# Kernel tuning notes

Measured on AMD Instinct MI355X. Metric: run time of the kernel, lower is better.

Reference implementation:

```python
import jax, jax.numpy as jnp
import numpy as np
from jax import lax

KERNEL = 3
EPS = 0.01


def _box_sum(x, k):
    # sum over kxk window, stride 1, SAME-style explicit padding of k//2
    pad = k // 2
    return lax.reduce_window(
        x, 0.0, lax.add,
        window_dimensions=(1, 1, k, k),
        window_strides=(1, 1, 1, 1),
        padding=((0, 0), (0, 0), (pad, pad), (pad, pad)),
    )


def _box_counts(h, w, k, dtype):
    # number of valid (non-padded) elements in each window (count_include_pad=False)
    ones = jnp.ones((1, 1, h, w), dtype=dtype)
    return _box_sum(ones, k)


def _blur(x, counts, k):
    return _box_sum(x, k) / counts


def setup_inputs() -> dict:
    key = jax.random.key(0)
    k1, k2 = jax.random.split(key)
    shape = (8, 16, 512, 512)
    inp = jax.random.normal(k1, shape, dtype=jnp.float32)
    guide = jax.random.normal(k2, shape, dtype=jnp.float32)
    return {"input": inp, "guide": guide}


def reference(input, guide):
    I, p = input, guide
    B, C, H, W = I.shape
    counts = _box_counts(H, W, KERNEL, I.dtype)  # [1,1,H,W]

    mean_I = _blur(I, counts, KERNEL)
    mean_p = _blur(p, counts, KERNEL)
    mean_II = _blur(I * I, counts, KERNEL)
    mean_Ip = _blur(I * p, counts, KERNEL)

    var_I = mean_II - mean_I * mean_I
    cov_Ip = mean_Ip - mean_I * mean_p

    a = cov_Ip / (var_I + EPS)
    b = mean_p - a * mean_I

    mean_a = _blur(a, counts, KERNEL)
    mean_b = _blur(b, counts, KERNEL)

    return mean_a * I + mean_b
```

## Files before the change

kernel.cpp:

```cpp
#include <hip/hip_runtime.h>


constexpr int W  = 512;
constexpr int H  = 512;
constexpr int TW = 64;
constexpr int TH = 16;
constexpr int ABH = TH + 2;
constexpr int ABW = TW + 2;
constexpr float EPS  = 0.01f;
constexpr float INV9 = 1.0f / 9.0f;

template<bool INT>
__device__ __forceinline__ void run_tile(
    const float* __restrict__ Ibase, const float* __restrict__ Pbase,
    float* __restrict__ Obase, int x0, int y0, int tid,
    float2 (*sAB)[ABW])
{
    if (tid < 198) {
        const int s   = tid / 33;
        const int p   = tid - 33 * s;
        const int ay0 = 3 * s;
        const int gx  = x0 - 2 + 2 * p;
        const int gy0 = y0 - 2 + ay0;

        float hI[2][3], hP[2][3], hII[2][3], hIP[2][3];
        #pragma unroll
        for (int j = 0; j < 5; ++j) {
            const int gy = gy0 + j;
            float i0, i1, i2, i3, q0, q1, q2, q3;
            if (INT) {
                const int g = gy * W + gx;
                const float2 a01 = *(const float2*)(Ibase + g);
                const float2 a23 = *(const float2*)(Ibase + g + 2);
                const float2 b01 = *(const float2*)(Pbase + g);
                const float2 b23 = *(const float2*)(Pbase + g + 2);
                i0 = a01.x; i1 = a01.y; i2 = a23.x; i3 = a23.y;
                q0 = b01.x; q1 = b01.y; q2 = b23.x; q3 = b23.y;
            } else {
                i0 = i1 = i2 = i3 = 0.f; q0 = q1 = q2 = q3 = 0.f;
                if ((unsigned)gy < (unsigned)H) {
                    const float* Ir = Ibase + gy * W;
                    const float* Pr = Pbase + gy * W;
                    if (gx >= 0 && gx + 3 < W) {
                        const float2 a01 = *(const float2*)(Ir + gx);
                        const float2 a23 = *(const float2*)(Ir + gx + 2);
                        const float2 b01 = *(const float2*)(Pr + gx);
                        const float2 b23 = *(const float2*)(Pr + gx + 2);
                        i0 = a01.x; i1 = a01.y; i2 = a23.x; i3 = a23.y;
                        q0 = b01.x; q1 = b01.y; q2 = b23.x; q3 = b23.y;
                    } else {
                        if ((unsigned)(gx + 0) < (unsigned)W) { i0 = Ir[gx + 0]; q0 = Pr[gx + 0]; }
                        if ((unsigned)(gx + 1) < (unsigned)W) { i1 = Ir[gx + 1]; q1 = Pr[gx + 1]; }
                        if ((unsigned)(gx + 2) < (unsigned)W) { i2 = Ir[gx + 2]; q2 = Pr[gx + 2]; }
                        if ((unsigned)(gx + 3) < (unsigned)W) { i3 = Ir[gx + 3]; q3 = Pr[gx + 3]; }
                    }
                }
            }
            const int k = j % 3;
            const float tI  = i1 + i2, tP = q1 + q2;
            const float tII = fmaf(i1, i1, i2 * i2);
            const float tIP = fmaf(i1, q1, i2 * q2);
            hI[0][k]  = tI + i0;            hI[1][k]  = tI + i3;
            hP[0][k]  = tP + q0;            hP[1][k]  = tP + q3;
            hII[0][k] = fmaf(i0, i0, tII);  hII[1][k] = fmaf(i3, i3, tII);
            hIP[0][k] = fmaf(i0, q0, tIP);  hIP[1][k] = fmaf(i3, q3, tIP);
            if (j >= 2) {
                const int ay = ay0 + j - 2;
                float ab[4];
                #pragma unroll
                for (int c = 0; c < 2; ++c) {
                    const float wI  = hI[c][0]  + hI[c][1]  + hI[c][2];
                    const float wP  = hP[c][0]  + hP[c][1]  + hP[c][2];
                    const float wII = hII[c][0] + hII[c][1] + hII[c][2];
                    const float wIP = hIP[c][0] + hIP[c][1] + hIP[c][2];
                    float a = 0.f, b = 0.f;
                    if (INT) {
                        const float mI   = wI * INV9, mP = wP * INV9;
                        const float varI = fmaf(-mI, mI, wII * INV9);
                        const float cov  = fmaf(-mI, mP, wIP * INV9);
                        a = cov * __builtin_amdgcn_rcpf(varI + EPS);
                        b = fmaf(-a, mI, mP);
                    } else {
                        const int axg = x0 - 1 + 2 * p + c;
                        const int ayg = y0 - 1 + ay;
                        if ((unsigned)axg < (unsigned)W && (unsigned)ayg < (unsigned)H) {
                            const float cx = 3.f - (float)(axg == 0) - (float)(axg == W - 1);
                            const float cy = 3.f - (float)(ayg == 0) - (float)(ayg == H - 1);
                            const float inv  = __builtin_amdgcn_rcpf(cx * cy);
                            const float mI   = wI * inv, mP = wP * inv;
                            const float varI = fmaf(-mI, mI, wII * inv);
                            const float cov  = fmaf(-mI, mP, wIP * inv);
                            a = cov * __builtin_amdgcn_rcpf(varI + EPS);
                            b = fmaf(-a, mI, mP);
                        }
                    }
                    ab[2 * c] = a; ab[2 * c + 1] = b;
                }
                *(float4*)&sAB[ay][2 * p] = make_float4(ab[0], ab[1], ab[2], ab[3]);
            }
        }
    }
    __syncthreads();

    {
        const int q   = tid & 31;
        const int r   = tid >> 5;
        const int ox0 = 2 * q;
        const int oy0 = 2 * r;
        float hA[2][3], hB[2][3];
        #pragma unroll
        for (int j = 0; j < 4; ++j) {
            const float4 c01 = *(const float4*)&sAB[oy0 + j][ox0];
            const float4 c23 = *(const float4*)&sAB[oy0 + j][ox0 + 2];
            const float a0 = c01.x, b0 = c01.y, a1 = c01.z, b1 = c01.w;
            const float a2 = c23.x, b2 = c23.y, a3 = c23.z, b3 = c23.w;
            const int k = j % 3;
            const float tA = a1 + a2, tB = b1 + b2;
            hA[0][k] = tA + a0; hA[1][k] = tA + a3;
            hB[0][k] = tB + b0; hB[1][k] = tB + b3;
            if (j >= 2) {
                const int oy = oy0 + j - 2;
                const int gy = y0 + oy;
                const int go = gy * W + x0 + ox0;
                const float2 iv = *(const float2*)(Ibase + go);
                float res[2];
                #pragma unroll
                for (int c = 0; c < 2; ++c) {
                    const float sa = hA[c][0] + hA[c][1] + hA[c][2];
                    const float sb = hB[c][0] + hB[c][1] + hB[c][2];
                    float inv;
                    if (INT) {
                        inv = INV9;
                    } else {
                        const int gxo = x0 + ox0 + c;
                        const float cx = 3.f - (float)(gxo == 0) - (float)(gxo == W - 1);
                        const float cy = 3.f - (float)(gy == 0) - (float)(gy == H - 1);
                        inv = __builtin_amdgcn_rcpf(cx * cy);
                    }
                    const float Ic = (c == 0) ? iv.x : iv.y;
                    res[c] = fmaf(sa * inv, Ic, sb * inv);
                }
                *(float2*)(Obase + go) = make_float2(res[0], res[1]);
            }
        }
    }
}

__global__ __launch_bounds__(256, 8) void guide_filter_kernel(
    const float* __restrict__ I, const float* __restrict__ P,
    float* __restrict__ O)
{
    __shared__ __align__(16) float2 sAB[ABH][ABW];

    const int tid = threadIdx.x;
    const int x0  = blockIdx.x * TW;
    const int y0  = blockIdx.y * TH;
    const size_t img_off = (size_t)blockIdx.z * (size_t)(W * H);
    const bool interior = (blockIdx.x > 0) & (blockIdx.x < gridDim.x - 1) &
                          (blockIdx.y > 0) & (blockIdx.y < gridDim.y - 1);
    if (interior) {
        run_tile<true >(I + img_off, P + img_off, (float*)O + img_off, x0, y0, tid, sAB);
    } else {
        run_tile<false>(I + img_off, P + img_off, (float*)O + img_off, x0, y0, tid, sAB);
    }
}

extern "C" void kernel_launch(void* const* d_in, const int* in_sizes, int n_in,
                              void* d_out, int out_size, void* d_ws, size_t ws_size,
                              hipStream_t stream) {
    const float* I = (const float*)d_in[0];
    const float* P = (const float*)d_in[1];
    float*       O = (float*)d_out;
    const int images = in_sizes[0] / (W * H);
    dim3 grid(W / TW, H / TH, images);
    guide_filter_kernel<<<grid, dim3(256), 0, stream>>>(I, P, O);
}
```

Measured before the change: 358.2 us.

## Replace shared-memory tiles with register-streaming column strips using wave shuffles

Each wavefront now processes a 128-column strip (120 output columns) and streams 64 rows downward, keeping rolling 3-row box sums for the statistics and for a/b in registers. Horizontal neighbours come from lane shuffles instead of a shared-memory tile, which removes the LDS staging, the block barrier and most halo re-reads. In exchange the grid is much smaller, there is a long serial per-row dependency chain, and the shuffles and boundary masks add per-row work.

```diff
diff --git a/kernel.cpp b/kernel.cpp
--- a/kernel.cpp
+++ b/kernel.cpp
@@ -1,168 +1,115 @@
 #include <hip/hip_runtime.h>
 
 
-constexpr int W  = 512;
-constexpr int H  = 512;
-constexpr int TW = 64;
-constexpr int TH = 16;
-constexpr int ABH = TH + 2;
-constexpr int ABW = TW + 2;
-constexpr float EPS  = 0.01f;
-constexpr float INV9 = 1.0f / 9.0f;
+constexpr int W = 512, H = 512;
+constexpr int OUTW = 120;
+constexpr int RG_H = 64;
+constexpr float EPS = 0.01f;
 
-template<bool INT>
-__device__ __forceinline__ void run_tile(
-    const float* __restrict__ Ibase, const float* __restrict__ Pbase,
-    float* __restrict__ Obase, int x0, int y0, int tid,
-    float2 (*sAB)[ABW])
-{
-    if (tid < 198) {
-        const int s   = tid / 33;
-        const int p   = tid - 33 * s;
-        const int ay0 = 3 * s;
-        const int gx  = x0 - 2 + 2 * p;
-        const int gy0 = y0 - 2 + ay0;
+#define GF_AB_COL(cx, wI, wP, wII, wIP, aa, bb)                               \
+    {                                                                         \
+        const float inv = __builtin_amdgcn_rcpf((cx) * cyA);                  \
+        const float mI = (wI) * inv, mP = (wP) * inv;                         \
+        const float varI = fmaf(-mI, mI, (wII) * inv);                        \
+        const float cov  = fmaf(-mI, mP, (wIP) * inv);                        \
+        aa = cov * __builtin_amdgcn_rcpf(varI + EPS);                         \
+        bb = fmaf(-aa, mI, mP);                                               \
+    }
 
-        float hI[2][3], hP[2][3], hII[2][3], hIP[2][3];
-        #pragma unroll
-        for (int j = 0; j < 5; ++j) {
-            const int gy = gy0 + j;
-            float i0, i1, i2, i3, q0, q1, q2, q3;
-            if (INT) {
-                const int g = gy * W + gx;
-                const float2 a01 = *(const float2*)(Ibase + g);
-                const float2 a23 = *(const float2*)(Ibase + g + 2);
-                const float2 b01 = *(const float2*)(Pbase + g);
-                const float2 b23 = *(const float2*)(Pbase + g + 2);
-                i0 = a01.x; i1 = a01.y; i2 = a23.x; i3 = a23.y;
-                q0 = b01.x; q1 = b01.y; q2 = b23.x; q3 = b23.y;
-            } else {
-                i0 = i1 = i2 = i3 = 0.f; q0 = q1 = q2 = q3 = 0.f;
-                if ((unsigned)gy < (unsigned)H) {
-                    const float* Ir = Ibase + gy * W;
-                    const float* Pr = Pbase + gy * W;
-                    if (gx >= 0 && gx + 3 < W) {
-                        const float2 a01 = *(const float2*)(Ir + gx);
-                        const float2 a23 = *(const float2*)(Ir + gx + 2);
-                        const float2 b01 = *(const float2*)(Pr + gx);
-                        const float2 b23 = *(const float2*)(Pr + gx + 2);
-                        i0 = a01.x; i1 = a01.y; i2 = a23.x; i3 = a23.y;
-                        q0 = b01.x; q1 = b01.y; q2 = b23.x; q3 = b23.y;
-                    } else {
-                        if ((unsigned)(gx + 0) < (unsigned)W) { i0 = Ir[gx + 0]; q0 = Pr[gx + 0]; }
-                        if ((unsigned)(gx + 1) < (unsigned)W) { i1 = Ir[gx + 1]; q1 = Pr[gx + 1]; }
-                        if ((unsigned)(gx + 2) < (unsigned)W) { i2 = Ir[gx + 2]; q2 = Pr[gx + 2]; }
-                        if ((unsigned)(gx + 3) < (unsigned)W) { i3 = Ir[gx + 3]; q3 = Pr[gx + 3]; }
-                    }
-                }
-            }
-            const int k = j % 3;
-            const float tI  = i1 + i2, tP = q1 + q2;
-            const float tII = fmaf(i1, i1, i2 * i2);
-            const float tIP = fmaf(i1, q1, i2 * q2);
-            hI[0][k]  = tI + i0;            hI[1][k]  = tI + i3;
-            hP[0][k]  = tP + q0;            hP[1][k]  = tP + q3;
-            hII[0][k] = fmaf(i0, i0, tII);  hII[1][k] = fmaf(i3, i3, tII);
-            hIP[0][k] = fmaf(i0, q0, tIP);  hIP[1][k] = fmaf(i3, q3, tIP);
-            if (j >= 2) {
-                const int ay = ay0 + j - 2;
-                float ab[4];
-                #pragma unroll
-                for (int c = 0; c < 2; ++c) {
-                    const float wI  = hI[c][0]  + hI[c][1]  + hI[c][2];
-                    const float wP  = hP[c][0]  + hP[c][1]  + hP[c][2];
-                    const float wII = hII[c][0] + hII[c][1] + hII[c][2];
-                    const float wIP = hIP[c][0] + hIP[c][1] + hIP[c][2];
-                    float a = 0.f, b = 0.f;
-                    if (INT) {
-                        const float mI   = wI * INV9, mP = wP * INV9;
-                        const float varI = fmaf(-mI, mI, wII * INV9);
-                        const float cov  = fmaf(-mI, mP, wIP * INV9);
-                        a = cov * __builtin_amdgcn_rcpf(varI + EPS);
-                        b = fmaf(-a, mI, mP);
-                    } else {
-                        const int axg = x0 - 1 + 2 * p + c;
-                        const int ayg = y0 - 1 + ay;
-                        if ((unsigned)axg < (unsigned)W && (unsigned)ayg < (unsigned)H) {
-                            const float cx = 3.f - (float)(axg == 0) - (float)(axg == W - 1);
-                            const float cy = 3.f - (float)(ayg == 0) - (float)(ayg == H - 1);
-                            const float inv  = __builtin_amdgcn_rcpf(cx * cy);
-                            const float mI   = wI * inv, mP = wP * inv;
-                            const float varI = fmaf(-mI, mI, wII * inv);
-                            const float cov  = fmaf(-mI, mP, wIP * inv);
-                            a = cov * __builtin_amdgcn_rcpf(varI + EPS);
-                            b = fmaf(-a, mI, mP);
-                        }
-                    }
-                    ab[2 * c] = a; ab[2 * c + 1] = b;
-                }
-                *(float4*)&sAB[ay][2 * p] = make_float4(ab[0], ab[1], ab[2], ab[3]);
-            }
-        }
-    }
-    __syncthreads();
+#define GF_STEP(r, S, SP1)                                                    \
+  {                                                                           \
+    const int gy = oy0 - 2 + (r);                                             \
+    const bool yok = (unsigned)gy < (unsigned)H;                              \
+    float ix = 0.f, iy = 0.f, px = 0.f, py = 0.f;                             \
+    if (xok & yok) {                                                          \
+        const float2 vi = *(const float2*)(Ib + gy * W + c0);                 \
+        const float2 vp = *(const float2*)(Pb + gy * W + c0);                 \
+        ix = vi.x; iy = vi.y; px = vp.x; py = vp.y;                           \
+    }                                                                         \
+    const float iLy = __shfl(iy, lm1);                                        \
+    const float pLy = __shfl(py, lm1);                                        \
+    const float iRx = __shfl(ix, lp1);                                        \
+    const float pRx = __shfl(px, lp1);                                        \
+    const float cI = ix + iy, cP = px + py;                                   \
+    hI0[S] = cI + iLy;  hI1[S] = cI + iRx;                                    \
+    hP0[S] = cP + pLy;  hP1[S] = cP + pRx;                                    \
+    const float cII = fmaf(ix, ix, iy * iy);                                  \
+    const float cIP = fmaf(ix, px, iy * py);                                  \
+    hII0[S] = fmaf(iLy, iLy, cII);  hII1[S] = fmaf(iRx, iRx, cII);            \
+    hIP0[S] = fmaf(iLy, pLy, cIP);  hIP1[S] = fmaf(iRx, pRx, cIP);            \
+    iC0[S] = ix; iC1[S] = iy;                                                 \
+    const int ay = gy - 1;                                                    \
+    const float cyA = 3.f - (float)(ay == 0) - (float)(ay == H - 1);          \
+    const bool abok = xok & ((unsigned)ay < (unsigned)H);                     \
+    float a0, b0, a1, b1;                                                     \
+    GF_AB_COL(cx0, hI0[0] + hI0[1] + hI0[2], hP0[0] + hP0[1] + hP0[2],        \
+              hII0[0] + hII0[1] + hII0[2], hIP0[0] + hIP0[1] + hIP0[2],       \
+              a0, b0)                                                         \
+    GF_AB_COL(cx1, hI1[0] + hI1[1] + hI1[2], hP1[0] + hP1[1] + hP1[2],        \
+              hII1[0] + hII1[1] + hII1[2], hIP1[0] + hIP1[1] + hIP1[2],       \
+              a1, b1)                                                         \
+    a0 = abok ? a0 : 0.f;  b0 = abok ? b0 : 0.f;                              \
+    a1 = abok ? a1 : 0.f;  b1 = abok ? b1 : 0.f;                              \
+    const float aLy = __shfl(a1, lm1);                                        \
+    const float bLy = __shfl(b1, lm1);                                        \
+    const float aRx = __shfl(a0, lp1);                                        \
+    const float bRx = __shfl(b0, lp1);                                        \
+    const float cA = a0 + a1, cB = b0 + b1;                                   \
+    hA0[S] = cA + aLy;  hA1[S] = cA + aRx;                                    \
+    hB0[S] = cB + bLy;  hB1[S] = cB + bRx;                                    \
+    if ((r) >= 4) {                                                           \
+        const int oy = gy - 2;                                                \
+        const float cyO = 3.f - (float)(oy == 0) - (float)(oy == H - 1);      \
+        const float q0 = __builtin_amdgcn_rcpf(cx0 * cyO);                    \
+        const float q1 = __builtin_amdgcn_rcpf(cx1 * cyO);                    \
+        const float sA0 = hA0[0] + hA0[1] + hA0[2];                           \
+        const float sB0 = hB0[0] + hB0[1] + hB0[2];                           \
+        const float sA1 = hA1[0] + hA1[1] + hA1[2];                           \
+        const float sB1 = hB1[0] + hB1[1] + hB1[2];                           \
+        const float o0 = fmaf(sA0 * q0, iC0[SP1], sB0 * q0);                  \
+        const float o1 = fmaf(sA1 * q1, iC1[SP1], sB1 * q1);                  \
+        if (stok) *(float2*)(Ob + oy * W + c0) = make_float2(o0, o1);         \
+    }                                                                         \
+  }
 
-    {
-        const int q   = tid & 31;
-        const int r   = tid >> 5;
-        const int ox0 = 2 * q;
-        const int oy0 = 2 * r;
-        float hA[2][3], hB[2][3];
-        #pragma unroll
-        for (int j = 0; j < 4; ++j) {
-            const float4 c01 = *(const float4*)&sAB[oy0 + j][ox0];
-            const float4 c23 = *(const float4*)&sAB[oy0 + j][ox0 + 2];
-            const float a0 = c01.x, b0 = c01.y, a1 = c01.z, b1 = c01.w;
-            const float a2 = c23.x, b2 = c23.y, a3 = c23.z, b3 = c23.w;
-            const int k = j % 3;
-            const float tA = a1 + a2, tB = b1 + b2;
-            hA[0][k] = tA + a0; hA[1][k] = tA + a3;
-            hB[0][k] = tB + b0; hB[1][k] = tB + b3;
-            if (j >= 2) {
-                const int oy = oy0 + j - 2;
-                const int gy = y0 + oy;
-                const int go = gy * W + x0 + ox0;
-                const float2 iv = *(const float2*)(Ibase + go);
-                float res[2];
-                #pragma unroll
-                for (int c = 0; c < 2; ++c) {
-                    const float sa = hA[c][0] + hA[c][1] + hA[c][2];
-                    const float sb = hB[c][0] + hB[c][1] + hB[c][2];
-                    float inv;
-                    if (INT) {
-                        inv = INV9;
-                    } else {
-                        const int gxo = x0 + ox0 + c;
-                        const float cx = 3.f - (float)(gxo == 0) - (float)(gxo == W - 1);
-                        const float cy = 3.f - (float)(gy == 0) - (float)(gy == H - 1);
-                        inv = __builtin_amdgcn_rcpf(cx * cy);
-                    }
-                    const float Ic = (c == 0) ? iv.x : iv.y;
-                    res[c] = fmaf(sa * inv, Ic, sb * inv);
-                }
-                *(float2*)(Obase + go) = make_float2(res[0], res[1]);
-            }
-        }
-    }
-}
-
-__global__ __launch_bounds__(256, 8) void guide_filter_kernel(
+__global__ __launch_bounds__(256, 4) void guide_filter_kernel(
     const float* __restrict__ I, const float* __restrict__ P,
     float* __restrict__ O)
 {
-    __shared__ __align__(16) float2 sAB[ABH][ABW];
+    const int lane = threadIdx.x & 63;
+    const int wid  = threadIdx.x >> 6;
+    const int band = blockIdx.x;
+    const int rg   = blockIdx.y * 4 + wid;
+    const size_t img_off = (size_t)blockIdx.z * (size_t)(W * H);
+    const float* Ib = I + img_off;
+    const float* Pb = P + img_off;
+    float*       Ob = O + img_off;
 
-    const int tid = threadIdx.x;
-    const int x0  = blockIdx.x * TW;
-    const int y0  = blockIdx.y * TH;
-    const size_t img_off = (size_t)blockIdx.z * (size_t)(W * H);
-    const bool interior = (blockIdx.x > 0) & (blockIdx.x < gridDim.x - 1) &
-                          (blockIdx.y > 0) & (blockIdx.y < gridDim.y - 1);
-    if (interior) {
-        run_tile<true >(I + img_off, P + img_off, (float*)O + img_off, x0, y0, tid, sAB);
-    } else {
-        run_tile<false>(I + img_off, P + img_off, (float*)O + img_off, x0, y0, tid, sAB);
+    const int c0 = band * OUTW - 2 + 2 * lane;
+    const int c1 = c0 + 1;
+    const bool xok  = (unsigned)c0 < (unsigned)W;
+    const bool stok = xok & (lane >= 1) & (lane <= 60);
+    const float cx0 = 3.f - (float)(c0 == 0);
+    const float cx1 = 3.f - (float)(c1 == W - 1);
+    const int oy0 = rg * RG_H;
+    const int lm1 = lane - 1, lp1 = lane + 1;
+
+    float hI0[3], hI1[3], hP0[3], hP1[3], hII0[3], hII1[3], hIP0[3], hIP1[3];
+    float hA0[3], hA1[3], hB0[3], hB1[3], iC0[3], iC1[3];
+    #pragma unroll
+    for (int s = 0; s < 3; ++s) {
+        hI0[s]=hI1[s]=hP0[s]=hP1[s]=hII0[s]=hII1[s]=hIP0[s]=hIP1[s]=0.f;
+        hA0[s]=hA1[s]=hB0[s]=hB1[s]=iC0[s]=iC1[s]=0.f;
     }
+
+    for (int g = 0; g < 22; ++g) {
+        const int r = 3 * g;
+        GF_STEP(r,     0, 1)
+        GF_STEP(r + 1, 1, 2)
+        GF_STEP(r + 2, 2, 0)
+    }
+    GF_STEP(66, 0, 1)
+    GF_STEP(67, 1, 2)
 }
 
 extern "C" void kernel_launch(void* const* d_in, const int* in_sizes, int n_in,
@@ -172,6 +119,6 @@
     const float* P = (const float*)d_in[1];
     float*       O = (float*)d_out;
     const int images = in_sizes[0] / (W * H);
-    dim3 grid(W / TW, H / TH, images);
+    dim3 grid(5, 2, images);
     guide_filter_kernel<<<grid, dim3(256), 0, stream>>>(I, P, O);
 }
```

New measurement: 332.0 us. -7.3%, faster.

## Stage input halo in LDS and double-buffer across four horizontal tiles per block

Applied to the files above, without the earlier changes.

Each block now walks four consecutive 64-wide tiles. For each tile it loads the interleaved I/P halo into a double-buffered shared-memory array using clamped coalesced loads, and prefetches the next tile into registers while the current one is computed. Stage 2 reads from LDS instead of issuing overlapping global loads, which removes redundant global traffic and divergent boundary loads. In exchange the block uses more LDS and gets a smaller grid (launch bounds drop to 4), with added barriers per tile and possible occupancy loss.

```diff
diff --git a/kernel.cpp b/kernel.cpp
--- a/kernel.cpp
+++ b/kernel.cpp
@@ -1,61 +1,31 @@
 #include <hip/hip_runtime.h>
 
 
-constexpr int W  = 512;
-constexpr int H  = 512;
-constexpr int TW = 64;
-constexpr int TH = 16;
+constexpr int W  = 512, H = 512;
+constexpr int TW = 64,  TH = 16, NT = 4;
+constexpr int IPH = TH + 4;
+constexpr int IPW = TW + 4;
 constexpr int ABH = TH + 2;
 constexpr int ABW = TW + 2;
 constexpr float EPS  = 0.01f;
 constexpr float INV9 = 1.0f / 9.0f;
 
 template<bool INT>
-__device__ __forceinline__ void run_tile(
-    const float* __restrict__ Ibase, const float* __restrict__ Pbase,
-    float* __restrict__ Obase, int x0, int y0, int tid,
-    float2 (*sAB)[ABW])
+__device__ __forceinline__ void stage2(
+    const float2 (*sIPb)[IPW], float2 (*sAB)[ABW], int x0, int y0, int tid)
 {
     if (tid < 198) {
         const int s   = tid / 33;
         const int p   = tid - 33 * s;
         const int ay0 = 3 * s;
-        const int gx  = x0 - 2 + 2 * p;
-        const int gy0 = y0 - 2 + ay0;
-
         float hI[2][3], hP[2][3], hII[2][3], hIP[2][3];
         #pragma unroll
         for (int j = 0; j < 5; ++j) {
-            const int gy = gy0 + j;
-            float i0, i1, i2, i3, q0, q1, q2, q3;
-            if (INT) {
-                const int g = gy * W + gx;
-                const float2 a01 = *(const float2*)(Ibase + g);
-                const float2 a23 = *(const float2*)(Ibase + g + 2);
-                const float2 b01 = *(const float2*)(Pbase + g);
-                const float2 b23 = *(const float2*)(Pbase + g + 2);
-                i0 = a01.x; i1 = a01.y; i2 = a23.x; i3 = a23.y;
-                q0 = b01.x; q1 = b01.y; q2 = b23.x; q3 = b23.y;
-            } else {
-                i0 = i1 = i2 = i3 = 0.f; q0 = q1 = q2 = q3 = 0.f;
-                if ((unsigned)gy < (unsigned)H) {
-                    const float* Ir = Ibase + gy * W;
-                    const float* Pr = Pbase + gy * W;
-                    if (gx >= 0 && gx + 3 < W) {
-                        const float2 a01 = *(const float2*)(Ir + gx);
-                        const float2 a23 = *(const float2*)(Ir + gx + 2);
-                        const float2 b01 = *(const float2*)(Pr + gx);
-                        const float2 b23 = *(const float2*)(Pr + gx + 2);
-                        i0 = a01.x; i1 = a01.y; i2 = a23.x; i3 = a23.y;
-                        q0 = b01.x; q1 = b01.y; q2 = b23.x; q3 = b23.y;
-                    } else {
-                        if ((unsigned)(gx + 0) < (unsigned)W) { i0 = Ir[gx + 0]; q0 = Pr[gx + 0]; }
-                        if ((unsigned)(gx + 1) < (unsigned)W) { i1 = Ir[gx + 1]; q1 = Pr[gx + 1]; }
-                        if ((unsigned)(gx + 2) < (unsigned)W) { i2 = Ir[gx + 2]; q2 = Pr[gx + 2]; }
-                        if ((unsigned)(gx + 3) < (unsigned)W) { i3 = Ir[gx + 3]; q3 = Pr[gx + 3]; }
-                    }
-                }
-            }
+            const int rr = ay0 + j;
+            const float4 c01 = *(const float4*)&sIPb[rr][2 * p];
+            const float4 c23 = *(const float4*)&sIPb[rr][2 * p + 2];
+            const float i0 = c01.x, q0 = c01.y, i1 = c01.z, q1 = c01.w;
+            const float i2 = c23.x, q2 = c23.y, i3 = c23.z, q3 = c23.w;
             const int k = j % 3;
             const float tI  = i1 + i2, tP = q1 + q2;
             const float tII = fmaf(i1, i1, i2 * i2);
@@ -100,68 +70,135 @@
             }
         }
     }
-    __syncthreads();
-
-    {
-        const int q   = tid & 31;
-        const int r   = tid >> 5;
-        const int ox0 = 2 * q;
-        const int oy0 = 2 * r;
-        float hA[2][3], hB[2][3];
-        #pragma unroll
-        for (int j = 0; j < 4; ++j) {
-            const float4 c01 = *(const float4*)&sAB[oy0 + j][ox0];
-            const float4 c23 = *(const float4*)&sAB[oy0 + j][ox0 + 2];
-            const float a0 = c01.x, b0 = c01.y, a1 = c01.z, b1 = c01.w;
-            const float a2 = c23.x, b2 = c23.y, a3 = c23.z, b3 = c23.w;
-            const int k = j % 3;
-            const float tA = a1 + a2, tB = b1 + b2;
-            hA[0][k] = tA + a0; hA[1][k] = tA + a3;
-            hB[0][k] = tB + b0; hB[1][k] = tB + b3;
-            if (j >= 2) {
-                const int oy = oy0 + j - 2;
-                const int gy = y0 + oy;
-                const int go = gy * W + x0 + ox0;
-                const float2 iv = *(const float2*)(Ibase + go);
-                float res[2];
-                #pragma unroll
-                for (int c = 0; c < 2; ++c) {
-                    const float sa = hA[c][0] + hA[c][1] + hA[c][2];
-                    const float sb = hB[c][0] + hB[c][1] + hB[c][2];
-                    float inv;
-                    if (INT) {
-                        inv = INV9;
-                    } else {
-                        const int gxo = x0 + ox0 + c;
-                        const float cx = 3.f - (float)(gxo == 0) - (float)(gxo == W - 1);
-                        const float cy = 3.f - (float)(gy == 0) - (float)(gy == H - 1);
-                        inv = __builtin_amdgcn_rcpf(cx * cy);
-                    }
-                    const float Ic = (c == 0) ? iv.x : iv.y;
-                    res[c] = fmaf(sa * inv, Ic, sb * inv);
+}
+
+template<bool INT>
+__device__ __forceinline__ void stage3(
+    const float2 (*sAB)[ABW], const float* __restrict__ Ibase,
+    float* __restrict__ Obase, int x0, int y0, int tid)
+{
+    const int q   = tid & 31;
+    const int r   = tid >> 5;
+    const int ox0 = 2 * q;
+    const int oy0 = 2 * r;
+    float hA[2][3], hB[2][3];
+    #pragma unroll
+    for (int j = 0; j < 4; ++j) {
+        const float4 c01 = *(const float4*)&sAB[oy0 + j][ox0];
+        const float4 c23 = *(const float4*)&sAB[oy0 + j][ox0 + 2];
+        const float a0 = c01.x, b0 = c01.y, a1 = c01.z, b1 = c01.w;
+        const float a2 = c23.x, b2 = c23.y, a3 = c23.z, b3 = c23.w;
+        const int k = j % 3;
+        const float tA = a1 + a2, tB = b1 + b2;
+        hA[0][k] = tA + a0; hA[1][k] = tA + a3;
+        hB[0][k] = tB + b0; hB[1][k] = tB + b3;
+        if (j >= 2) {
+            const int oy = oy0 + j - 2;
+            const int gy = y0 + oy;
+            const int go = gy * W + x0 + ox0;
+            const float2 iv = *(const float2*)(Ibase + go);
+            float res[2];
+            #pragma unroll
+            for (int c = 0; c < 2; ++c) {
+                const float sa = hA[c][0] + hA[c][1] + hA[c][2];
+                const float sb = hB[c][0] + hB[c][1] + hB[c][2];
+                float inv;
+                if (INT) {
+                    inv = INV9;
+                } else {
+                    const int gxo = x0 + ox0 + c;
+                    const float cx = 3.f - (float)(gxo == 0) - (float)(gxo == W - 1);
+                    const float cy = 3.f - (float)(gy == 0) - (float)(gy == H - 1);
+                    inv = __builtin_amdgcn_rcpf(cx * cy);
                 }
-                *(float2*)(Obase + go) = make_float2(res[0], res[1]);
+                const float Ic = (c == 0) ? iv.x : iv.y;
+                res[c] = fmaf(sa * inv, Ic, sb * inv);
             }
-        }
-    }
-}
-
-__global__ __launch_bounds__(256, 8) void guide_filter_kernel(
+            *(float2*)(Obase + go) = make_float2(res[0], res[1]);
+        }
+    }
+}
+
+__global__ __launch_bounds__(256, 4) void guide_filter_kernel(
     const float* __restrict__ I, const float* __restrict__ P,
     float* __restrict__ O)
 {
+    __shared__ __align__(16) float2 sIP[2][IPH][IPW];
     __shared__ __align__(16) float2 sAB[ABH][ABW];
 
-    const int tid = threadIdx.x;
-    const int x0  = blockIdx.x * TW;
-    const int y0  = blockIdx.y * TH;
+    const int tid   = threadIdx.x;
+    const int y0    = blockIdx.y * TH;
+    const int xbase = blockIdx.x * (NT * TW);
     const size_t img_off = (size_t)blockIdx.z * (size_t)(W * H);
-    const bool interior = (blockIdx.x > 0) & (blockIdx.x < gridDim.x - 1) &
-                          (blockIdx.y > 0) & (blockIdx.y < gridDim.y - 1);
-    if (interior) {
-        run_tile<true >(I + img_off, P + img_off, (float*)O + img_off, x0, y0, tid, sAB);
-    } else {
-        run_tile<false>(I + img_off, P + img_off, (float*)O + img_off, x0, y0, tid, sAB);
+    const float* Ib = I + img_off;
+    const float* Pb = P + img_off;
+    float*       Ob = O + img_off;
+
+    int trow[3], tpc[3]; bool tval[3];
+    #pragma unroll
+    for (int k = 0; k < 3; ++k) {
+        const int task = tid + 256 * k;
+        tval[k] = task < 34 * IPH;
+        const int row = task / 34;
+        trow[k] = row;
+        tpc[k]  = task - 34 * row;
+    }
+
+    float2 rI[3], rP[3];
+    auto issue = [&](int x0n) {
+        #pragma unroll
+        for (int k = 0; k < 3; ++k) {
+            int gy = y0 - 2 + trow[k];
+            gy = gy < 0 ? 0 : (gy > H - 1 ? H - 1 : gy);
+            int gx = x0n - 2 + 2 * tpc[k];
+            gx = gx < 0 ? 0 : (gx > W - 2 ? W - 2 : gx);
+            const size_t off = (size_t)gy * W + gx;
+            rI[k] = *(const float2*)(Ib + off);
+            rP[k] = *(const float2*)(Pb + off);
+        }
+    };
+    auto commit = [&](float2 (*dst)[IPW], int x0n, bool intr) {
+        #pragma unroll
+        for (int k = 0; k < 3; ++k) {
+            if (!tval[k]) continue;
+            float i0 = rI[k].x, i1 = rI[k].y, q0 = rP[k].x, q1 = rP[k].y;
+            if (!intr) {
+                const int gy = y0 - 2 + trow[k];
+                const int gx = x0n - 2 + 2 * tpc[k];
+                const bool ry   = (unsigned)gy < (unsigned)H;
+                const bool c0ok = ry & ((unsigned)gx < (unsigned)W);
+                const bool c1ok = ry & ((unsigned)(gx + 1) < (unsigned)W);
+                i0 = c0ok ? i0 : 0.f;  q0 = c0ok ? q0 : 0.f;
+                i1 = c1ok ? i1 : 0.f;  q1 = c1ok ? q1 : 0.f;
+            }
+            *(float4*)&dst[trow[k]][2 * tpc[k]] = make_float4(i0, q0, i1, q1);
+        }
+    };
+
+    {
+        const int  x00   = xbase;
+        const bool intr0 = (x00 > 0) & (x00 < W - TW) & (y0 > 0) & (y0 < H - TH);
+        issue(x00);
+        commit(sIP[0], x00, intr0);
+    }
+
+    int buf = 0;
+    for (int t = 0; t < NT; ++t) {
+        const int  x0   = xbase + t * TW;
+        const bool intr = (x0 > 0) & (x0 < W - TW) & (y0 > 0) & (y0 < H - TH);
+        __syncthreads();
+        if (t < NT - 1) issue(x0 + TW);
+        if (intr) stage2<true >(sIP[buf], sAB, x0, y0, tid);
+        else      stage2<false>(sIP[buf], sAB, x0, y0, tid);
+        __syncthreads();
+        if (t < NT - 1) {
+            const int  x0n   = x0 + TW;
+            const bool intrn = (x0n > 0) & (x0n < W - TW) & (y0 > 0) & (y0 < H - TH);
+            commit(sIP[buf ^ 1], x0n, intrn);
+        }
+        if (intr) stage3<true >(sAB, Ib, Ob, x0, y0, tid);
+        else      stage3<false>(sAB, Ib, Ob, x0, y0, tid);
+        buf ^= 1;
     }
 }
 
@@ -172,6 +209,6 @@
     const float* P = (const float*)d_in[1];
     float*       O = (float*)d_out;
     const int images = in_sizes[0] / (W * H);
-    dim3 grid(W / TW, H / TH, images);
+    dim3 grid(W / (NT * TW), H / TH, images);
     guide_filter_kernel<<<grid, dim3(256), 0, stream>>>(I, P, O);
 }
```

Measured after the change: 327.3 us. 1.09x faster.
